# Performance work log

Hardware: AMD Instinct MI355X
Metric: run time of the kernel (lower is better)

Reference implementation:

```python
import jax, jax.numpy as jnp
import numpy as np

B, T, D, H = 4, 2048, 1024, 16
HD = D // H


def setup_inputs() -> dict:
    key = jax.random.key(0)
    ks = jax.random.split(key, 10)
    s = 1.0 / np.sqrt(D)
    # xavier_uniform bound for wbias [T,T]: sqrt(6/(T+T))
    wb_bound = float(np.sqrt(6.0 / (T + T)))
    return {
        "x": jax.random.normal(ks[0], (B, T, D), dtype=jnp.float32),
        "Wq": jax.random.normal(ks[1], (D, D), dtype=jnp.float32) * s,
        "bq": jnp.zeros((D,), dtype=jnp.float32),
        "Wk": jax.random.normal(ks[2], (D, D), dtype=jnp.float32) * s,
        "bk": jnp.zeros((D,), dtype=jnp.float32),
        "Wv": jax.random.normal(ks[3], (D, D), dtype=jnp.float32) * s,
        "bv": jnp.zeros((D,), dtype=jnp.float32),
        "Wo": jax.random.normal(ks[4], (D, D), dtype=jnp.float32) * s,
        "bo": jnp.zeros((D,), dtype=jnp.float32),
        "wbias": jax.random.uniform(ks[5], (T, T), dtype=jnp.float32,
                                    minval=-wb_bound, maxval=wb_bound),
    }


def reference(x, Wq, bq, Wk, bk, Wv, bv, Wo, bo, wbias):
    Bc, Tc, Dc = x.shape
    # projections, split heads: [B, H, T, HD]
    def proj(W, b):
        y = x @ W + b
        return y.reshape(Bc, Tc, H, HD).transpose(0, 2, 1, 3)

    Q = proj(Wq, bq)
    K = proj(Wk, bk)
    V = proj(Wv, bv)

    Q_sig = jax.nn.sigmoid(Q)
    eK = jnp.exp(K)                      # [B,H,T,HD]
    ew = jnp.exp(wbias[:Tc, :Tc])        # [T,T]

    num = jnp.einsum('ts,bhsd->bhtd', ew, eK * V)
    den = jnp.einsum('ts,bhsd->bhtd', ew, eK)
    out = Q_sig * (num / den)            # [B,H,T,HD]

    out = out.transpose(0, 2, 1, 3).reshape(Bc, Tc, Dc)
    return out @ Wo + bo
```

## Files before the change

### kernel.cpp

```cpp
#include <hip/hip_runtime.h>
#include <hip/hip_bf16.h>


#define AS1(p) ((const __attribute__((address_space(1))) void*)(p))
#define AS3(p) ((__attribute__((address_space(3))) void*)(p))

typedef _Float16 half8 __attribute__((ext_vector_type(8)));
typedef _Float16 half4v __attribute__((ext_vector_type(4)));
typedef float floatx16 __attribute__((ext_vector_type(16)));
typedef int intx4 __attribute__((ext_vector_type(4)));
typedef int intx8 __attribute__((ext_vector_type(8)));

__device__ __forceinline__ long frag_off(int r, int k) {
  return (long)(((((r >> 5) * 4 + (k >> 4)) * 2 + ((k >> 3) & 1)) * 32 + (r & 31)) * 8 + (k & 7));
}
__device__ __forceinline__ long off8(int r, int k) {
  return (long)((((((r >> 5) * 2 + ((k >> 6) & 1)) * 2 + ((k >> 4) & 1)) * 2 + ((k >> 5) & 1)) * 32 +
                 (r & 31)) * 16 + (k & 15));
}

__global__ __launch_bounds__(256) void prep_all(
    const float* __restrict__ x, const float* __restrict__ wb, const float* __restrict__ Wq,
    const float* __restrict__ Wk, const float* __restrict__ Wv, const float* __restrict__ Wo,
    _Float16* __restrict__ x_h, char* __restrict__ E8, _Float16* __restrict__ WqkvT,
    _Float16* __restrict__ WoT) {
  __shared__ _Float16 lds[64 * 132];
  const int bid = blockIdx.x;
  const int tid = threadIdx.x;

  if (bid < 1024) {
    const int tm = bid >> 4, tk = bid & 15;
    const long tbase = (long)bid * 8192;
#pragma unroll
    for (int p = 0; p < 4; ++p) {
      const int s = p * 256 + tid;
      const int r = ((s >> 8) << 5) + (s & 31);
      const int k = ((s >> 6) & 3) * 16 + ((s >> 5) & 1) * 8;
      const float* sp = x + (long)(tm * 128 + r) * 1024 + tk * 64 + k;
      const float4 v0 = *(const float4*)sp;
      const float4 v1 = *(const float4*)(sp + 4);
      half8 h;
      h[0] = (_Float16)v0.x; h[1] = (_Float16)v0.y; h[2] = (_Float16)v0.z; h[3] = (_Float16)v0.w;
      h[4] = (_Float16)v1.x; h[5] = (_Float16)v1.y; h[6] = (_Float16)v1.z; h[7] = (_Float16)v1.w;
      *(half8*)(x_h + tbase + (long)s * 8) = h;
    }
    return;
  }

  if (bid >= 1536) {
    const int e = bid - 1536;
    const int tt = e >> 4, ts = e & 15;
    char* dst = E8 + (long)e * 16384;
#pragma unroll
    for (int p = 0; p < 16; ++p) {
      const int idx = p * 256 + tid;
      const int r = idx >> 5, k = (idx & 31) * 4;
      const float4 v = *(const float4*)(wb + (long)(tt * 128 + r) * 2048 + ts * 128 + k);
      const float e0 = (__expf(v.x) - 1.0f) * 32.0f, e1 = (__expf(v.y) - 1.0f) * 32.0f;
      const float e2 = (__expf(v.z) - 1.0f) * 32.0f, e3 = (__expf(v.w) - 1.0f) * 32.0f;
      int pk = __builtin_amdgcn_cvt_pk_fp8_f32(e0, e1, 0, false);
      pk = __builtin_amdgcn_cvt_pk_fp8_f32(e2, e3, pk, true);
      *(int*)(dst + off8(r, k)) = pk;
    }
    return;
  }

  const int b2 = bid - 1024;
  const float* src0;
  const float* src1 = nullptr;
  _Float16* dst;
  int tn, tk, cb = 0;
  if (b2 < 128) {
    tn = b2 >> 4; tk = b2 & 15; src0 = Wq; dst = WqkvT;
  } else if (b2 < 384) {
    const int t = b2 - 128;
    tn = 8 + (t >> 4); tk = t & 15; cb = (tn - 8) * 64; src0 = Wk; src1 = Wv; dst = WqkvT;
  } else {
    const int t = b2 - 384;
    tn = t >> 4; tk = t & 15; src0 = Wo; dst = WoT;
  }
  if (!src1) {
#pragma unroll
    for (int p = 0; p < 8; ++p) {
      const int kl = p * 8 + (tid >> 5);
      const int cl = (tid & 31) * 4;
      const float4 v = *(const float4*)(src0 + (long)(tk * 64 + kl) * 1024 + tn * 128 + cl);
      half4v h;
      h[0] = (_Float16)v.x; h[1] = (_Float16)v.y; h[2] = (_Float16)v.z; h[3] = (_Float16)v.w;
      *(half4v*)(lds + kl * 132 + cl) = h;
    }
  } else {
#pragma unroll
    for (int m = 0; m < 2; ++m) {
      const float* s = m ? src1 : src0;
      const int rb = m ? 32 : 0;
#pragma unroll
      for (int p = 0; p < 4; ++p) {
        const int kl = p * 16 + (tid >> 4);
        const int cl = (tid & 15) * 4;
        const int rl = (cl >> 5) * 64 + rb + (cl & 31);
        const float4 v = *(const float4*)(s + (long)(tk * 64 + kl) * 1024 + cb + cl);
        half4v h;
        h[0] = (_Float16)v.x; h[1] = (_Float16)v.y; h[2] = (_Float16)v.z; h[3] = (_Float16)v.w;
        *(half4v*)(lds + kl * 132 + rl) = h;
      }
    }
  }
  __syncthreads();
  const long tbase = (long)(tn * 16 + tk) * 8192;
#pragma unroll
  for (int p = 0; p < 4; ++p) {
    const int s = p * 256 + tid;
    const int r = ((s >> 8) << 5) + (s & 31);
    const int kl = ((s >> 6) & 3) * 16 + ((s >> 5) & 1) * 8;
    half8 h;
#pragma unroll
    for (int j = 0; j < 8; ++j) h[j] = lds[(kl + j) * 132 + r];
    *(half8*)(dst + tbase + (long)s * 8) = h;
  }
}

template <int VM>
__device__ __forceinline__ void aft_phase(int g, const _Float16* __restrict__ Ablk,
                                          const _Float16* __restrict__ Bblk,
                                          _Float16* ring, int tid, int wid, int lane,
                                          int wm, int wn, floatx16 (&acc)[2][2]) {
  const _Float16* slotA = ring + (g & 3) * 4096;
  const _Float16* slotB = ring + 16384 + (g & 3) * 8192;
  half8 af[2][2], bf[2][2];
#pragma unroll
  for (int mt = 0; mt < 2; ++mt)
#pragma unroll
    for (int ks = 0; ks < 2; ++ks)
      af[mt][ks] = *(const half8*)(slotA + (((wm >> 5) + mt) * 2 + ks) * 512 + lane * 8);
#pragma unroll
  for (int nt = 0; nt < 2; ++nt)
#pragma unroll
    for (int ks = 0; ks < 2; ++ks)
      bf[nt][ks] = *(const half8*)(slotB + (((wn >> 5) + nt) * 2 + ks) * 512 + lane * 8);
  const int gs = g + 3;
  if (gs < 32) {
    const int t = gs >> 1;
    const long goff = (long)(tid >> 7) * 2048 + (gs & 1) * 1024 + (tid & 127) * 8;
    _Float16* dA = ring + (gs & 3) * 4096 + wid * 512;
    _Float16* dB = ring + 16384 + (gs & 3) * 8192 + wid * 512;
    __builtin_amdgcn_global_load_lds(AS1(Ablk + (long)t * 8192 + goff), AS3(dA), 16, 0, 0);
    __builtin_amdgcn_global_load_lds(AS1(Bblk + (long)t * 8192 + goff), AS3(dB), 16, 0, 0);
    __builtin_amdgcn_global_load_lds(AS1(Bblk + (long)(16 + t) * 8192 + goff), AS3(dB + 4096),
                                     16, 0, 0);
  }
  asm volatile("s_waitcnt vmcnt(%0)" ::"i"(VM) : "memory");
  __builtin_amdgcn_s_barrier();
  asm volatile("s_waitcnt lgkmcnt(0)" ::: "memory");
  __builtin_amdgcn_s_setprio(1);
#pragma unroll
  for (int ks = 0; ks < 2; ++ks)
#pragma unroll
    for (int mt = 0; mt < 2; ++mt)
#pragma unroll
      for (int nt = 0; nt < 2; ++nt)
        acc[mt][nt] =
            __builtin_amdgcn_mfma_f32_32x32x16_f16(af[mt][ks], bf[nt][ks], acc[mt][nt], 0, 0, 0);
  __builtin_amdgcn_s_setprio(0);
  __builtin_amdgcn_s_barrier();
  asm volatile("" ::: "memory");
}

template <int MODE>
__global__ __launch_bounds__(512, 2) void gemm_bt2(
    const _Float16* __restrict__ A, const _Float16* __restrict__ Bt, void* __restrict__ Cv,
    const float* __restrict__ bias0, const float* __restrict__ bias1,
    const float* __restrict__ bias2, char* __restrict__ Zt8, float* __restrict__ cs) {
  __shared__ __align__(16) _Float16 ring[49152];
  const int tid = threadIdx.x;
  const int wid = tid >> 6, lane = tid & 63;
  const int l32 = lane & 31, khalf = lane >> 5;

  const int f = blockIdx.x;
  const int j = f >> 3;
  const int bxs = (f & 7) * 8 + (j & 7);
  const int bys = j >> 3;
  const int m0 = bxs * 128, n0 = bys * 256;
  const int wm = (wid >> 2) * 64, wn = (wid & 3) * 64;

  const _Float16* Ablk = A + (long)bxs * 131072;
  const _Float16* Bblk = Bt + (long)(bys * 2) * 131072;

#pragma unroll
  for (int g0 = 0; g0 < 3; ++g0) {
    const int t = g0 >> 1;
    const long goff = (long)(tid >> 7) * 2048 + (g0 & 1) * 1024 + (tid & 127) * 8;
    __builtin_amdgcn_global_load_lds(AS1(Ablk + (long)t * 8192 + goff),
                                     AS3(ring + g0 * 4096 + wid * 512), 16, 0, 0);
    __builtin_amdgcn_global_load_lds(AS1(Bblk + (long)t * 8192 + goff),
                                     AS3(ring + 16384 + g0 * 8192 + wid * 512), 16, 0, 0);
    __builtin_amdgcn_global_load_lds(AS1(Bblk + (long)(16 + t) * 8192 + goff),
                                     AS3(ring + 16384 + g0 * 8192 + 4096 + wid * 512), 16, 0, 0);
  }
  asm volatile("s_waitcnt vmcnt(6)" ::: "memory");
  __builtin_amdgcn_s_barrier();
  asm volatile("" ::: "memory");

  floatx16 acc[2][2] = {};
#pragma unroll 1
  for (int gb = 0; gb < 28; gb += 4) {
    aft_phase<6>(gb + 0, Ablk, Bblk, ring, tid, wid, lane, wm, wn, acc);
    aft_phase<6>(gb + 1, Ablk, Bblk, ring, tid, wid, lane, wm, wn, acc);
    aft_phase<6>(gb + 2, Ablk, Bblk, ring, tid, wid, lane, wm, wn, acc);
    aft_phase<6>(gb + 3, Ablk, Bblk, ring, tid, wid, lane, wm, wn, acc);
  }
  aft_phase<6>(28, Ablk, Bblk, ring, tid, wid, lane, wm, wn, acc);
  aft_phase<3>(29, Ablk, Bblk, ring, tid, wid, lane, wm, wn, acc);
  aft_phase<0>(30, Ablk, Bblk, ring, tid, wid, lane, wm, wn, acc);
  aft_phase<0>(31, Ablk, Bblk, ring, tid, wid, lane, wm, wn, acc);

  if (MODE == 0) {
    if (n0 < 1024) {
      _Float16* Qs = (_Float16*)Cv;
#pragma unroll
      for (int mt = 0; mt < 2; ++mt) {
        const long ttile = (m0 + wm + mt * 32) >> 5;
#pragma unroll
        for (int nt = 0; nt < 2; ++nt) {
          const int col = n0 + wn + nt * 32 + l32;
          const float bb = bias0[col];
          const long base = (ttile * 32 + (((n0 + wn) >> 5) + nt)) * 1024;
#pragma unroll
          for (int q = 0; q < 4; ++q) {
            half4v o;
#pragma unroll
            for (int rr = 0; rr < 4; ++rr) {
              const float v = acc[mt][nt][q * 4 + rr] + bb;
              o[rr] = (_Float16)(1.0f / (1.0f + __expf(-v)));
            }
            *(half4v*)(Qs + base + q * 256 + lane * 4) = o;
          }
        }
      }
    } else {
      const int grp = (n0 - 1024 + wn) >> 6;
      const int ch = grp * 32 + l32;
      const float bkc = bias1[ch], bvc = bias2[ch];
      const int jn = grp * 64 + l32;
      const int b = m0 >> 11;
      char* Z8 = Zt8 + (long)b * 4194304 +
                 ((long)(jn >> 7) * 16 + ((m0 & 2047) >> 7)) * 16384;
      const int jnl = jn & 127;
      float sk = 0.f, sz = 0.f;
#pragma unroll
      for (int mt = 0; mt < 2; ++mt) {
#pragma unroll
        for (int q = 0; q < 4; ++q) {
          float ekv[4], ekk[4];
#pragma unroll
          for (int rr = 0; rr < 4; ++rr) {
            const float ek = __expf(acc[mt][0][q * 4 + rr] + bkc);
            const float vv = acc[mt][1][q * 4 + rr] + bvc;
            ekk[rr] = ek;
            ekv[rr] = ek * vv;
            sk += ek;
            sz += ek * vv;
          }
          const int sl = wm + mt * 32 + 4 * khalf + 8 * q;
          int pn = __builtin_amdgcn_cvt_pk_fp8_f32(ekv[0] * 0.25f, ekv[1] * 0.25f, 0, false);
          pn = __builtin_amdgcn_cvt_pk_fp8_f32(ekv[2] * 0.25f, ekv[3] * 0.25f, pn, true);
          int pd = __builtin_amdgcn_cvt_pk_fp8_f32(ekk[0] * 0.25f, ekk[1] * 0.25f, 0, false);
          pd = __builtin_amdgcn_cvt_pk_fp8_f32(ekk[2] * 0.25f, ekk[3] * 0.25f, pd, true);
          *(int*)(Z8 + off8(jnl, sl)) = pn;
          *(int*)(Z8 + off8(jnl + 32, sl)) = pd;
        }
      }
      atomicAdd(&cs[(long)b * 2048 + ch * 2], sz);
      atomicAdd(&cs[(long)b * 2048 + ch * 2 + 1], sk);
    }
    return;
  }

#pragma unroll
  for (int mt = 0; mt < 2; ++mt)
#pragma unroll
    for (int nt = 0; nt < 2; ++nt) {
      const int col = n0 + wn + nt * 32 + l32;
      const float bb = bias0[col];
#pragma unroll
      for (int reg = 0; reg < 16; ++reg) {
        const int row = m0 + wm + mt * 32 + 4 * khalf + 8 * (reg >> 2) + (reg & 3);
        ((float*)Cv)[(long)row * 1024 + col] = acc[mt][nt][reg] + bb;
      }
    }
}

template <int VM, bool STAGE, int SLOT>
__device__ __forceinline__ void g2_phase(int g, char* __restrict__ ringA, char* __restrict__ ringB,
                                         const char* At0, const char* At1,
                                         const char* Bt0, const char* Bt1,
                                         int tid, int lane, int wm, int wn,
                                         floatx16 (&acc)[2][4]) {
  const int l32 = lane & 31, khalf = lane >> 5;
  intx8 a8[2], b8[4];
#pragma unroll
  for (int mt = 0; mt < 2; ++mt) {
    const int G = (wm >> 5) + mt;
    const char* pa = ringA + SLOT * 16384 + (G >> 2) * 8192 + (G & 3) * 2048 + khalf * 512 + l32 * 16;
    const intx4 alo = *(const intx4*)pa;
    const intx4 ahi = *(const intx4*)(pa + 1024);
    a8[mt] = __builtin_shufflevector(alo, ahi, 0, 1, 2, 3, 4, 5, 6, 7);
  }
#pragma unroll
  for (int nt = 0; nt < 4; ++nt) {
    const int Gn = (wn >> 5) + nt;
    const char* pb = ringB + SLOT * 16384 + (Gn >> 2) * 8192 + (Gn & 3) * 2048 + khalf * 512 + l32 * 16;
    const intx4 blo = *(const intx4*)pb;
    const intx4 bhi = *(const intx4*)(pb + 1024);
    b8[nt] = __builtin_shufflevector(blo, bhi, 0, 1, 2, 3, 4, 5, 6, 7);
  }
  if (STAGE) {
    const int ks = g + 2;
    constexpr int SS = (SLOT + 2) % 3;
    const long gsrc = (long)(ks >> 1) * 16384 + (long)(tid >> 7) * 4096 + (long)(ks & 1) * 2048 +
                      (tid & 127) * 16;
    char* dA = ringA + SS * 16384 + tid * 16;
    char* dB = ringB + SS * 16384 + tid * 16;
    __builtin_amdgcn_global_load_lds(AS1(At0 + gsrc), AS3(dA), 16, 0, 0);
    __builtin_amdgcn_global_load_lds(AS1(At1 + gsrc), AS3(dA + 8192), 16, 0, 0);
    __builtin_amdgcn_global_load_lds(AS1(Bt0 + gsrc), AS3(dB), 16, 0, 0);
    __builtin_amdgcn_global_load_lds(AS1(Bt1 + gsrc), AS3(dB + 8192), 16, 0, 0);
  }
  if constexpr (VM >= 0) {
    asm volatile("s_waitcnt vmcnt(%0)" ::"i"(VM) : "memory");
    __builtin_amdgcn_s_barrier();
  }
  asm volatile("s_waitcnt lgkmcnt(0)" ::: "memory");
  __builtin_amdgcn_s_setprio(1);
#pragma unroll
  for (int mt = 0; mt < 2; ++mt)
#pragma unroll
    for (int nt = 0; nt < 4; ++nt)
      acc[mt][nt] = __builtin_amdgcn_mfma_scale_f32_32x32x64_f8f6f4(
          a8[mt], b8[nt], acc[mt][nt], 0, 0, 0, 127u, 0, 127u);
  __builtin_amdgcn_s_setprio(0);
  if constexpr (VM >= 0) {
    __builtin_amdgcn_s_barrier();
    asm volatile("" ::: "memory");
  }
}

__global__ __launch_bounds__(512, 1) void gemm2_fp8(
    const char* __restrict__ E8, const char* __restrict__ Zt8, _Float16* __restrict__ OH,
    const _Float16* __restrict__ Qsig, const float* __restrict__ cs) {
  __shared__ __align__(16) char ring[98304];
  char* ringA = ring;
  char* ringB = ring + 49152;
  const int tid = threadIdx.x;
  const int wid = tid >> 6, lane = tid & 63;
  const int l32 = lane & 31, khalf = lane >> 5;

  const int f = blockIdx.x;
  const int bxs = f & 7;
  const int bys = (f >> 3) & 7;
  const int bzs = f >> 6;
  const int m0 = bxs * 256;
  const int wm = (wid >> 1) * 64, wn = (wid & 1) * 128;

  const char* At0 = E8 + (long)(bxs * 2) * 262144;
  const char* At1 = At0 + 262144;
  const char* Bt0 = Zt8 + (long)bzs * 4194304 + (long)(bys * 2) * 262144;
  const char* Bt1 = Bt0 + 262144;

#pragma unroll
  for (int ks = 0; ks < 2; ++ks) {
    const long gsrc = (long)(tid >> 7) * 4096 + (long)(ks & 1) * 2048 + (tid & 127) * 16;
    char* dA = ringA + ks * 16384 + tid * 16;
    char* dB = ringB + ks * 16384 + tid * 16;
    __builtin_amdgcn_global_load_lds(AS1(At0 + gsrc), AS3(dA), 16, 0, 0);
    __builtin_amdgcn_global_load_lds(AS1(At1 + gsrc), AS3(dA + 8192), 16, 0, 0);
    __builtin_amdgcn_global_load_lds(AS1(Bt0 + gsrc), AS3(dB), 16, 0, 0);
    __builtin_amdgcn_global_load_lds(AS1(Bt1 + gsrc), AS3(dB + 8192), 16, 0, 0);
  }
  asm volatile("s_waitcnt vmcnt(4)" ::: "memory");
  __builtin_amdgcn_s_barrier();
  asm volatile("" ::: "memory");

  floatx16 acc[2][4] = {};
#pragma unroll 1
  for (int gb = 0; gb < 30; gb += 3) {
    g2_phase<4, true, 0>(gb + 0, ringA, ringB, At0, At1, Bt0, Bt1, tid, lane, wm, wn, acc);
    g2_phase<4, true, 1>(gb + 1, ringA, ringB, At0, At1, Bt0, Bt1, tid, lane, wm, wn, acc);
    g2_phase<4, true, 2>(gb + 2, ringA, ringB, At0, At1, Bt0, Bt1, tid, lane, wm, wn, acc);
  }
  g2_phase<0, false, 0>(30, ringA, ringB, At0, At1, Bt0, Bt1, tid, lane, wm, wn, acc);
  g2_phase<-1, false, 1>(31, ringA, ringB, At0, At1, Bt0, Bt1, tid, lane, wm, wn, acc);

  const int g32b = bys * 4 + (wn >> 6);
#pragma unroll
  for (int mt = 0; mt < 2; ++mt) {
    const long ttile = (long)(bzs * 2048 + m0 + wm + mt * 32) >> 5;
#pragma unroll
    for (int p = 0; p < 2; ++p) {
      const int g32 = g32b + p;
      const int ch = g32 * 32 + l32;
      const float2 c2 = *(const float2*)(cs + (long)bzs * 2048 + ch * 2);
      const long qbase = (ttile * 32 + g32) * 1024;
#pragma unroll
      for (int q = 0; q < 4; ++q) {
        const half4v qv = *(const half4v*)(Qsig + qbase + q * 256 + lane * 4);
#pragma unroll
        for (int rr = 0; rr < 4; ++rr) {
          const int reg = q * 4 + rr;
          const float num = c2.x + acc[mt][2 * p][reg] * 0.125f;
          const float den = c2.y + acc[mt][2 * p + 1][reg] * 0.125f;
          const int r = m0 + wm + mt * 32 + 4 * khalf + 8 * q + rr;
          const int R = bzs * 2048 + r;
          const long off = ((long)(R >> 7) * 16 + (ch >> 6)) * 8192 + frag_off(R & 127, ch & 63);
          OH[off] = (_Float16)((float)qv[rr] * num / den);
        }
      }
    }
  }
}

extern "C" void kernel_launch(void* const* d_in, const int* in_sizes, int n_in, void* d_out,
                              int out_size, void* d_ws, size_t ws_size, hipStream_t stream) {
  const float* x = (const float*)d_in[0];
  const float* Wq = (const float*)d_in[1];
  const float* bq = (const float*)d_in[2];
  const float* Wk = (const float*)d_in[3];
  const float* bk = (const float*)d_in[4];
  const float* Wv = (const float*)d_in[5];
  const float* bv = (const float*)d_in[6];
  const float* Wo = (const float*)d_in[7];
  const float* bo = (const float*)d_in[8];
  const float* wb = (const float*)d_in[9];

  char* ws = (char*)d_ws;
  _Float16* x_h = (_Float16*)(ws + 0);
  _Float16* WqkvT = (_Float16*)(ws + 16777216);
  _Float16* WoT = (_Float16*)(ws + 23068672);
  char* E8 = (char*)(ws + 25165824);
  _Float16* Qsig = (_Float16*)(ws + 29360128);
  char* Zt8 = (char*)(ws + 46137344);
  _Float16* OutHead = (_Float16*)(ws + 62914560);
  float* cs = (float*)(ws + 79691776);

  hipMemsetAsync(cs, 0, 4 * 2048 * sizeof(float), stream);

  prep_all<<<1792, 256, 0, stream>>>(x, wb, Wq, Wk, Wv, Wo, x_h, E8, WqkvT, WoT);

  gemm_bt2<0><<<768, 512, 0, stream>>>(x_h, WqkvT, Qsig, bq, bk, bv, Zt8, cs);

  gemm2_fp8<<<256, 512, 0, stream>>>(E8, Zt8, OutHead, Qsig, cs);

  gemm_bt2<2><<<256, 512, 0, stream>>>(OutHead, WoT, d_out, bo, nullptr, nullptr, nullptr, nullptr);
}
```

Measured before the change: 246.7 us.

## Software-pipeline LDS fragment reads one stage ahead and drop second barrier in GEMM

The GEMM main loop now double-buffers register fragments: each phase reads the next stage's A/B fragments from LDS after the barrier while the MFMAs consume the current fragments. The trailing barrier per phase is removed and the vmcnt/lgkmcnt waits are merged, so there is one barrier per k-step instead of two. The main loop is also fully unrolled. This raises register pressure (two fragment sets) and relies on the 4-slot ring plus the three-stage lookahead to keep the global-to-LDS writes from overwriting slots that are still being read.

```diff
diff --git a/kernel.cpp b/kernel.cpp
--- a/kernel.cpp
+++ b/kernel.cpp
@@ -120,26 +120,15 @@
   }
 }
 
-template <int VM>
-__device__ __forceinline__ void aft_phase(int g, const _Float16* __restrict__ Ablk,
-                                          const _Float16* __restrict__ Bblk,
-                                          _Float16* ring, int tid, int wid, int lane,
-                                          int wm, int wn, floatx16 (&acc)[2][2]) {
-  const _Float16* slotA = ring + (g & 3) * 4096;
-  const _Float16* slotB = ring + 16384 + (g & 3) * 8192;
-  half8 af[2][2], bf[2][2];
-#pragma unroll
-  for (int mt = 0; mt < 2; ++mt)
-#pragma unroll
-    for (int ks = 0; ks < 2; ++ks)
-      af[mt][ks] = *(const half8*)(slotA + (((wm >> 5) + mt) * 2 + ks) * 512 + lane * 8);
-#pragma unroll
-  for (int nt = 0; nt < 2; ++nt)
-#pragma unroll
-    for (int ks = 0; ks < 2; ++ks)
-      bf[nt][ks] = *(const half8*)(slotB + (((wn >> 5) + nt) * 2 + ks) * 512 + lane * 8);
-  const int gs = g + 3;
-  if (gs < 32) {
+template <int VM, bool STAGE, bool RDNEXT>
+__device__ __forceinline__ void aft_p(int g, const _Float16* __restrict__ Ablk,
+                                      const _Float16* __restrict__ Bblk, _Float16* ring,
+                                      int tid, int wid, int lane, int wm, int wn,
+                                      half8 (&curA)[2][2], half8 (&curB)[2][2],
+                                      half8 (&nxtA)[2][2], half8 (&nxtB)[2][2],
+                                      floatx16 (&acc)[2][2]) {
+  if (STAGE) {
+    const int gs = g + 3;
     const int t = gs >> 1;
     const long goff = (long)(tid >> 7) * 2048 + (gs & 1) * 1024 + (tid & 127) * 8;
     _Float16* dA = ring + (gs & 3) * 4096 + wid * 512;
@@ -149,9 +138,24 @@
     __builtin_amdgcn_global_load_lds(AS1(Bblk + (long)(16 + t) * 8192 + goff), AS3(dB + 4096),
                                      16, 0, 0);
   }
-  asm volatile("s_waitcnt vmcnt(%0)" ::"i"(VM) : "memory");
-  __builtin_amdgcn_s_barrier();
-  asm volatile("s_waitcnt lgkmcnt(0)" ::: "memory");
+  if constexpr (VM >= 0) {
+    asm volatile("s_waitcnt vmcnt(%0) lgkmcnt(0)" ::"i"(VM) : "memory");
+    __builtin_amdgcn_s_barrier();
+  }
+  if (RDNEXT) {
+    const _Float16* sA = ring + ((g + 1) & 3) * 4096 + lane * 8;
+    const _Float16* sB = ring + 16384 + ((g + 1) & 3) * 8192 + lane * 8;
+#pragma unroll
+    for (int mt = 0; mt < 2; ++mt)
+#pragma unroll
+      for (int ks = 0; ks < 2; ++ks)
+        nxtA[mt][ks] = *(const half8*)(sA + (((wm >> 5) + mt) * 2 + ks) * 512);
+#pragma unroll
+    for (int nt = 0; nt < 2; ++nt)
+#pragma unroll
+      for (int ks = 0; ks < 2; ++ks)
+        nxtB[nt][ks] = *(const half8*)(sB + (((wn >> 5) + nt) * 2 + ks) * 512);
+  }
   __builtin_amdgcn_s_setprio(1);
 #pragma unroll
   for (int ks = 0; ks < 2; ++ks)
@@ -160,10 +164,8 @@
 #pragma unroll
       for (int nt = 0; nt < 2; ++nt)
         acc[mt][nt] =
-            __builtin_amdgcn_mfma_f32_32x32x16_f16(af[mt][ks], bf[nt][ks], acc[mt][nt], 0, 0, 0);
+            __builtin_amdgcn_mfma_f32_32x32x16_f16(curA[mt][ks], curB[nt][ks], acc[mt][nt], 0, 0, 0);
   __builtin_amdgcn_s_setprio(0);
-  __builtin_amdgcn_s_barrier();
-  asm volatile("" ::: "memory");
 }
 
 template <int MODE>
@@ -201,18 +203,32 @@
   __builtin_amdgcn_s_barrier();
   asm volatile("" ::: "memory");
 
+  half8 fA0[2][2], fB0[2][2], fA1[2][2], fB1[2][2];
+  {
+    const _Float16* sA = ring + lane * 8;
+    const _Float16* sB = ring + 16384 + lane * 8;
+#pragma unroll
+    for (int mt = 0; mt < 2; ++mt)
+#pragma unroll
+      for (int ks = 0; ks < 2; ++ks)
+        fA0[mt][ks] = *(const half8*)(sA + (((wm >> 5) + mt) * 2 + ks) * 512);
+#pragma unroll
+    for (int nt = 0; nt < 2; ++nt)
+#pragma unroll
+      for (int ks = 0; ks < 2; ++ks)
+        fB0[nt][ks] = *(const half8*)(sB + (((wn >> 5) + nt) * 2 + ks) * 512);
+  }
+
   floatx16 acc[2][2] = {};
-#pragma unroll 1
-  for (int gb = 0; gb < 28; gb += 4) {
-    aft_phase<6>(gb + 0, Ablk, Bblk, ring, tid, wid, lane, wm, wn, acc);
-    aft_phase<6>(gb + 1, Ablk, Bblk, ring, tid, wid, lane, wm, wn, acc);
-    aft_phase<6>(gb + 2, Ablk, Bblk, ring, tid, wid, lane, wm, wn, acc);
-    aft_phase<6>(gb + 3, Ablk, Bblk, ring, tid, wid, lane, wm, wn, acc);
-  }
-  aft_phase<6>(28, Ablk, Bblk, ring, tid, wid, lane, wm, wn, acc);
-  aft_phase<3>(29, Ablk, Bblk, ring, tid, wid, lane, wm, wn, acc);
-  aft_phase<0>(30, Ablk, Bblk, ring, tid, wid, lane, wm, wn, acc);
-  aft_phase<0>(31, Ablk, Bblk, ring, tid, wid, lane, wm, wn, acc);
+#pragma unroll
+  for (int gb = 0; gb < 28; gb += 2) {
+    aft_p<6, true, true>(gb + 0, Ablk, Bblk, ring, tid, wid, lane, wm, wn, fA0, fB0, fA1, fB1, acc);
+    aft_p<6, true, true>(gb + 1, Ablk, Bblk, ring, tid, wid, lane, wm, wn, fA1, fB1, fA0, fB0, acc);
+  }
+  aft_p<6, true, true>(28, Ablk, Bblk, ring, tid, wid, lane, wm, wn, fA0, fB0, fA1, fB1, acc);
+  aft_p<3, false, true>(29, Ablk, Bblk, ring, tid, wid, lane, wm, wn, fA1, fB1, fA0, fB0, acc);
+  aft_p<0, false, true>(30, Ablk, Bblk, ring, tid, wid, lane, wm, wn, fA0, fB0, fA1, fB1, acc);
+  aft_p<-1, false, false>(31, Ablk, Bblk, ring, tid, wid, lane, wm, wn, fA1, fB1, fA0, fB0, acc);
 
   if (MODE == 0) {
     if (n0 < 1024) {
```

Result: no change. 250.1 us (+1.4%).

## Restructure GEMM mainloop into 64-wide K tiles with register double-buffered LDS reads

Applied to the files above, without the earlier changes.

The GEMM mainloop moves from 32-wide K phases in a 4-slot ring to 64-wide K tiles in a 3-slot ring, with one barrier per tile instead of two per phase. LDS fragment reads are double-buffered in registers so the next k-slice is read while the current MFMAs run, and the first fragment of the next tile is loaded right after the barrier. The intent is to hide LDS latency and cut barrier overhead. In exchange LDS use grows to 144KB and launch bounds drop to one block per CU, which lowers occupancy.

```diff
diff --git a/kernel.cpp b/kernel.cpp
--- a/kernel.cpp
+++ b/kernel.cpp
@@ -120,58 +120,70 @@
   }
 }
 
-template <int VM>
-__device__ __forceinline__ void aft_phase(int g, const _Float16* __restrict__ Ablk,
-                                          const _Float16* __restrict__ Bblk,
-                                          _Float16* ring, int tid, int wid, int lane,
-                                          int wm, int wn, floatx16 (&acc)[2][2]) {
-  const _Float16* slotA = ring + (g & 3) * 4096;
-  const _Float16* slotB = ring + 16384 + (g & 3) * 8192;
-  half8 af[2][2], bf[2][2];
+template <int KS>
+__device__ __forceinline__ void rd_ab(const _Float16* sA, const _Float16* sB, int wm, int wn,
+                                      int lane, half8 (&a)[2], half8 (&b)[2]) {
+  a[0] = *(const half8*)(sA + (((wm >> 5) + 0) * 4 + KS) * 512 + lane * 8);
+  a[1] = *(const half8*)(sA + (((wm >> 5) + 1) * 4 + KS) * 512 + lane * 8);
+  b[0] = *(const half8*)(sB + (((wn >> 5) + 0) * 4 + KS) * 512 + lane * 8);
+  b[1] = *(const half8*)(sB + (((wn >> 5) + 1) * 4 + KS) * 512 + lane * 8);
+}
+
+__device__ __forceinline__ void mm4(const half8 (&a)[2], const half8 (&b)[2],
+                                    floatx16 (&acc)[2][2]) {
+  __builtin_amdgcn_s_setprio(1);
 #pragma unroll
   for (int mt = 0; mt < 2; ++mt)
 #pragma unroll
-    for (int ks = 0; ks < 2; ++ks)
-      af[mt][ks] = *(const half8*)(slotA + (((wm >> 5) + mt) * 2 + ks) * 512 + lane * 8);
-#pragma unroll
-  for (int nt = 0; nt < 2; ++nt)
-#pragma unroll
-    for (int ks = 0; ks < 2; ++ks)
-      bf[nt][ks] = *(const half8*)(slotB + (((wn >> 5) + nt) * 2 + ks) * 512 + lane * 8);
-  const int gs = g + 3;
-  if (gs < 32) {
-    const int t = gs >> 1;
-    const long goff = (long)(tid >> 7) * 2048 + (gs & 1) * 1024 + (tid & 127) * 8;
-    _Float16* dA = ring + (gs & 3) * 4096 + wid * 512;
-    _Float16* dB = ring + 16384 + (gs & 3) * 8192 + wid * 512;
-    __builtin_amdgcn_global_load_lds(AS1(Ablk + (long)t * 8192 + goff), AS3(dA), 16, 0, 0);
-    __builtin_amdgcn_global_load_lds(AS1(Bblk + (long)t * 8192 + goff), AS3(dB), 16, 0, 0);
-    __builtin_amdgcn_global_load_lds(AS1(Bblk + (long)(16 + t) * 8192 + goff), AS3(dB + 4096),
-                                     16, 0, 0);
-  }
-  asm volatile("s_waitcnt vmcnt(%0)" ::"i"(VM) : "memory");
-  __builtin_amdgcn_s_barrier();
-  asm volatile("s_waitcnt lgkmcnt(0)" ::: "memory");
-  __builtin_amdgcn_s_setprio(1);
-#pragma unroll
-  for (int ks = 0; ks < 2; ++ks)
-#pragma unroll
-    for (int mt = 0; mt < 2; ++mt)
-#pragma unroll
-      for (int nt = 0; nt < 2; ++nt)
-        acc[mt][nt] =
-            __builtin_amdgcn_mfma_f32_32x32x16_f16(af[mt][ks], bf[nt][ks], acc[mt][nt], 0, 0, 0);
+    for (int nt = 0; nt < 2; ++nt)
+      acc[mt][nt] = __builtin_amdgcn_mfma_f32_32x32x16_f16(a[mt], b[nt], acc[mt][nt], 0, 0, 0);
   __builtin_amdgcn_s_setprio(0);
-  __builtin_amdgcn_s_barrier();
-  asm volatile("" ::: "memory");
+}
+
+template <int VM, bool STAGE, bool LAST>
+__device__ __forceinline__ void tile_step(int t, const _Float16* __restrict__ Ablk,
+                                          const _Float16* __restrict__ Bblk, _Float16* ring,
+                                          int tid, int lane, int wm, int wn,
+                                          half8 (&a0)[2], half8 (&b0)[2], half8 (&a1)[2],
+                                          half8 (&b1)[2], floatx16 (&acc)[2][2]) {
+  const _Float16* sA = ring + (t % 3) * 8192;
+  const _Float16* sB = ring + 24576 + (t % 3) * 16384;
+  if (STAGE) {
+    const int ts = t + 2;
+    _Float16* dA = ring + (ts % 3) * 8192 + tid * 8;
+    _Float16* dB = ring + 24576 + (ts % 3) * 16384 + tid * 8;
+    const _Float16* gA = Ablk + (long)ts * 8192 + tid * 8;
+    const _Float16* gB = Bblk + (long)ts * 8192 + tid * 8;
+    __builtin_amdgcn_global_load_lds(AS1(gA), AS3(dA), 16, 0, 0);
+    __builtin_amdgcn_global_load_lds(AS1(gA + 4096), AS3(dA + 4096), 16, 0, 0);
+    __builtin_amdgcn_global_load_lds(AS1(gB), AS3(dB), 16, 0, 0);
+    __builtin_amdgcn_global_load_lds(AS1(gB + 4096), AS3(dB + 4096), 16, 0, 0);
+    __builtin_amdgcn_global_load_lds(AS1(gB + 131072), AS3(dB + 8192), 16, 0, 0);
+    __builtin_amdgcn_global_load_lds(AS1(gB + 131072 + 4096), AS3(dB + 12288), 16, 0, 0);
+  }
+  rd_ab<1>(sA, sB, wm, wn, lane, a1, b1);
+  mm4(a0, b0, acc);
+  rd_ab<2>(sA, sB, wm, wn, lane, a0, b0);
+  mm4(a1, b1, acc);
+  rd_ab<3>(sA, sB, wm, wn, lane, a1, b1);
+  mm4(a0, b0, acc);
+  if (!LAST) {
+    asm volatile("s_waitcnt vmcnt(%0)" ::"i"(VM < 0 ? 0 : VM) : "memory");
+    __builtin_amdgcn_s_barrier();
+    asm volatile("" ::: "memory");
+    const _Float16* nA = ring + ((t + 1) % 3) * 8192;
+    const _Float16* nB = ring + 24576 + ((t + 1) % 3) * 16384;
+    rd_ab<0>(nA, nB, wm, wn, lane, a0, b0);
+  }
+  mm4(a1, b1, acc);
 }
 
 template <int MODE>
-__global__ __launch_bounds__(512, 2) void gemm_bt2(
+__global__ __launch_bounds__(512, 1) void gemm_bt2(
     const _Float16* __restrict__ A, const _Float16* __restrict__ Bt, void* __restrict__ Cv,
     const float* __restrict__ bias0, const float* __restrict__ bias1,
     const float* __restrict__ bias2, char* __restrict__ Zt8, float* __restrict__ cs) {
-  __shared__ __align__(16) _Float16 ring[49152];
+  __shared__ __align__(16) _Float16 ring[73728];
   const int tid = threadIdx.x;
   const int wid = tid >> 6, lane = tid & 63;
   const int l32 = lane & 31, khalf = lane >> 5;
@@ -187,32 +199,31 @@
   const _Float16* Bblk = Bt + (long)(bys * 2) * 131072;
 
 #pragma unroll
-  for (int g0 = 0; g0 < 3; ++g0) {
-    const int t = g0 >> 1;
-    const long goff = (long)(tid >> 7) * 2048 + (g0 & 1) * 1024 + (tid & 127) * 8;
-    __builtin_amdgcn_global_load_lds(AS1(Ablk + (long)t * 8192 + goff),
-                                     AS3(ring + g0 * 4096 + wid * 512), 16, 0, 0);
-    __builtin_amdgcn_global_load_lds(AS1(Bblk + (long)t * 8192 + goff),
-                                     AS3(ring + 16384 + g0 * 8192 + wid * 512), 16, 0, 0);
-    __builtin_amdgcn_global_load_lds(AS1(Bblk + (long)(16 + t) * 8192 + goff),
-                                     AS3(ring + 16384 + g0 * 8192 + 4096 + wid * 512), 16, 0, 0);
+  for (int t0 = 0; t0 < 2; ++t0) {
+    _Float16* dA = ring + t0 * 8192 + tid * 8;
+    _Float16* dB = ring + 24576 + t0 * 16384 + tid * 8;
+    const _Float16* gA = Ablk + (long)t0 * 8192 + tid * 8;
+    const _Float16* gB = Bblk + (long)t0 * 8192 + tid * 8;
+    __builtin_amdgcn_global_load_lds(AS1(gA), AS3(dA), 16, 0, 0);
+    __builtin_amdgcn_global_load_lds(AS1(gA + 4096), AS3(dA + 4096), 16, 0, 0);
+    __builtin_amdgcn_global_load_lds(AS1(gB), AS3(dB), 16, 0, 0);
+    __builtin_amdgcn_global_load_lds(AS1(gB + 4096), AS3(dB + 4096), 16, 0, 0);
+    __builtin_amdgcn_global_load_lds(AS1(gB + 131072), AS3(dB + 8192), 16, 0, 0);
+    __builtin_amdgcn_global_load_lds(AS1(gB + 131072 + 4096), AS3(dB + 12288), 16, 0, 0);
   }
   asm volatile("s_waitcnt vmcnt(6)" ::: "memory");
   __builtin_amdgcn_s_barrier();
   asm volatile("" ::: "memory");
 
+  half8 a0[2], b0[2], a1[2], b1[2];
+  rd_ab<0>(ring, ring + 24576, wm, wn, lane, a0, b0);
+
   floatx16 acc[2][2] = {};
-#pragma unroll 1
-  for (int gb = 0; gb < 28; gb += 4) {
-    aft_phase<6>(gb + 0, Ablk, Bblk, ring, tid, wid, lane, wm, wn, acc);
-    aft_phase<6>(gb + 1, Ablk, Bblk, ring, tid, wid, lane, wm, wn, acc);
-    aft_phase<6>(gb + 2, Ablk, Bblk, ring, tid, wid, lane, wm, wn, acc);
-    aft_phase<6>(gb + 3, Ablk, Bblk, ring, tid, wid, lane, wm, wn, acc);
-  }
-  aft_phase<6>(28, Ablk, Bblk, ring, tid, wid, lane, wm, wn, acc);
-  aft_phase<3>(29, Ablk, Bblk, ring, tid, wid, lane, wm, wn, acc);
-  aft_phase<0>(30, Ablk, Bblk, ring, tid, wid, lane, wm, wn, acc);
-  aft_phase<0>(31, Ablk, Bblk, ring, tid, wid, lane, wm, wn, acc);
+#pragma unroll
+  for (int t = 0; t < 14; ++t)
+    tile_step<6, true, false>(t, Ablk, Bblk, ring, tid, lane, wm, wn, a0, b0, a1, b1, acc);
+  tile_step<0, false, false>(14, Ablk, Bblk, ring, tid, lane, wm, wn, a0, b0, a1, b1, acc);
+  tile_step<0, false, true>(15, Ablk, Bblk, ring, tid, lane, wm, wn, a0, b0, a1, b1, acc);
 
   if (MODE == 0) {
     if (n0 < 1024) {
```

Result: no change. 247.3 us (+0.2%).
